# Performance work log

Measured on AMD Instinct MI355X. Metric: run time of the kernel, lower is better.

## Reference

```python
import jax, jax.numpy as jnp
import numpy as np

HIDDEN = 64
N_IN = 5
N_APP = 4
DT = 0.1
EPS = 1e-5  # torch LayerNorm default
N_HEAD_TYPES = 5  # p, q1, q3, q5, q7


def _layernorm(x, w, b):
    mu = jnp.mean(x, axis=-1, keepdims=True)
    var = jnp.mean((x - mu) ** 2, axis=-1, keepdims=True)
    return (x - mu) * jax.lax.rsqrt(var + EPS) * w + b


def setup_inputs() -> dict:
    key = jax.random.key(0)
    ks = jax.random.split(key, 8)
    B, T = 4096, 2048
    x = jax.random.normal(ks[0], (B, T, N_IN), dtype=jnp.float32)
    # xavier_uniform for rec_weights
    lim_rec = float(np.sqrt(6.0 / (HIDDEN + HIDDEN)))
    W_rec = jax.random.uniform(ks[1], (HIDDEN, HIDDEN), jnp.float32, -lim_rec, lim_rec)
    # nn.Linear default init: U(-1/sqrt(fan_in), 1/sqrt(fan_in))
    lim_in = float(np.sqrt(1.0 / N_IN))
    W_in = jax.random.uniform(ks[2], (N_IN, HIDDEN), jnp.float32, -lim_in, lim_in)
    b_in = jax.random.uniform(ks[3], (HIDDEN,), jnp.float32, -lim_in, lim_in)
    tau_param = jnp.ones((HIDDEN,), jnp.float32)
    ln1_w = jnp.ones((HIDDEN,), jnp.float32)
    ln1_b = jnp.zeros((HIDDEN,), jnp.float32)
    ln2_w = jnp.ones((HIDDEN,), jnp.float32)
    ln2_b = jnp.zeros((HIDDEN,), jnp.float32)
    lim_h = float(np.sqrt(1.0 / HIDDEN))
    head_W = jax.random.uniform(ks[4], (N_HEAD_TYPES, N_APP, HIDDEN), jnp.float32, -lim_h, lim_h)
    head_b = jax.random.uniform(ks[5], (N_HEAD_TYPES, N_APP), jnp.float32, -lim_h, lim_h)
    return {"x": x, "W_in": W_in, "b_in": b_in, "tau_param": tau_param,
            "W_rec": W_rec, "ln1_w": ln1_w, "ln1_b": ln1_b,
            "ln2_w": ln2_w, "ln2_b": ln2_b, "head_W": head_W, "head_b": head_b}


def reference(x, W_in, b_in, tau_param, W_rec, ln1_w, ln1_b, ln2_w, ln2_b, head_W, head_b):
    B = x.shape[0]
    tau = jax.nn.softplus(tau_param)  # (H,)
    # precompute the input projection for all timesteps: (T, B, H)
    xw = jnp.einsum('bts,sh->tbh', x, W_in) + b_in

    def step(h, xt):
        f = jnp.tanh(_layernorm(xt + h @ W_rec, ln1_w, ln1_b))
        h = jnp.clip(h + (-h / tau + f) * DT, -10.0, 10.0)
        return h, None

    h0 = jnp.zeros((B, HIDDEN), x.dtype)
    h, _ = jax.lax.scan(step, h0, xw)
    h = _layernorm(h, ln2_w, ln2_b)
    # stacked heads: row 0 = p_out, rows 1..4 = q1, q3, q5, q7  -> (5, B, n_app)
    out = jnp.einsum('bh,kah->kba', h, head_W) + head_b[:, None, :]
    return out
```

## Files before the change

kernel.cpp:

```cpp
#include <hip/hip_runtime.h>

#define HIDDEN  64
#define T_STEPS 2048
#define N_INPUT 5
#define DT      0.1f
#define LN_EPS  1e-5f
#define ROWS    16
#define TANH_K  2.885390081777927f

typedef short bf16x8 __attribute__((ext_vector_type(8)));
typedef float f32x4  __attribute__((ext_vector_type(4)));

union FragU { uint4 u4; unsigned int u[4]; unsigned short us[8]; bf16x8 v; };

__device__ __forceinline__ unsigned short bf16_trunc(float f) {
    return (unsigned short)(__float_as_uint(f) >> 16);
}
__device__ __forceinline__ float bf16_hi_f32(float f) {
    return __uint_as_float(__float_as_uint(f) & 0xFFFF0000u);
}
__device__ __forceinline__ unsigned int pack_hi2(float f0, float f1) {
    return __builtin_amdgcn_perm(__float_as_uint(f1), __float_as_uint(f0), 0x07060302u);
}

#define MFMA(A, B, C) __builtin_amdgcn_mfma_f32_16x16x32_bf16((A), (B), (C), 0, 0, 0)

__global__ __launch_bounds__(256, 1) void hlnn_mfma4(
    const float* __restrict__ x, const float* __restrict__ W_in,
    const float* __restrict__ b_in, const float* __restrict__ tau_param,
    const float* __restrict__ W_rec, const float* __restrict__ ln1_w,
    const float* __restrict__ ln1_b, const float* __restrict__ ln2_w,
    const float* __restrict__ ln2_b, const float* __restrict__ head_W,
    const float* __restrict__ head_b, float* __restrict__ out, int Btot)
{
    const int tid  = threadIdx.x;
    const int lane = tid & 63;
    const int w    = tid >> 6;
    const int r    = lane & 15;
    const int q    = lane >> 4;
    const int g    = blockIdx.x;

    __shared__ unsigned short hHi[ROWS][72];
    __shared__ unsigned short hLo[ROWS][72];
    __shared__ float2 stats2[ROWS][18];
    __shared__ float  hnbuf[ROWS][68];

    FragU A_hi[2], A_lo[2];
    const int cfrag = 16 * w + r;
#pragma unroll
    for (int kk = 0; kk < 2; ++kk)
#pragma unroll
        for (int j = 0; j < 8; ++j) {
            const float wv = W_rec[(kk * 32 + q * 8 + j) * HIDDEN + cfrag];
            A_hi[kk].us[j] = bf16_trunc(wv);
            A_lo[kk].us[j] = bf16_trunc(wv - bf16_hi_f32(wv));
        }
    FragU Ax_hi, Ax_lo;
#pragma unroll
    for (int j = 0; j < 8; ++j) {
        const int kg = q * 8 + j;
        const float wv = (kg < N_INPUT) ? W_in[kg * HIDDEN + cfrag] : 0.0f;
        Ax_hi.us[j] = bf16_trunc(wv);
        Ax_lo.us[j] = bf16_trunc(wv - bf16_hi_f32(wv));
    }

    float w1K[4], b1K[4], dec4[4], ln2w4[4], ln2b4[4];
    f32x4 cinit;
#pragma unroll
    for (int e = 0; e < 4; ++e) {
        const int c = 16 * w + 4 * q + e;
        w1K[e]  = ln1_w[c] * TANH_K;
        b1K[e]  = ln1_b[c] * TANH_K;
        const float tp  = tau_param[c];
        const float tau = (tp > 20.0f) ? tp : log1pf(expf(tp));
        dec4[e]  = 1.0f - DT / tau;
        ln2w4[e] = ln2_w[c];  ln2b4[e] = ln2_b[c];
        cinit[e] = b_in[c];
    }

    const float* xrow = x + (size_t)(g * ROWS + r) * T_STEPS * N_INPUT;

    f32x4 accx;
    {
        const float x0 = xrow[0], x1 = xrow[1], x2 = xrow[2], x3 = xrow[3], x4 = xrow[4];
        FragU BxH, BxL;
        BxH.u[0] = pack_hi2(x0, x1); BxH.u[1] = pack_hi2(x2, x3);
        BxH.u[2] = pack_hi2(x4, 0.f); BxH.u[3] = 0u;
        BxL.u[0] = pack_hi2(x0 - bf16_hi_f32(x0), x1 - bf16_hi_f32(x1));
        BxL.u[1] = pack_hi2(x2 - bf16_hi_f32(x2), x3 - bf16_hi_f32(x3));
        BxL.u[2] = pack_hi2(x4 - bf16_hi_f32(x4), 0.f); BxL.u[3] = 0u;
        accx = MFMA(Ax_hi.v, BxH.v, cinit);
        accx = MFMA(Ax_hi.v, BxL.v, accx);
        accx = MFMA(Ax_lo.v, BxH.v, accx);
    }

    FragU Bh[2], Bl[2];
    Bh[0].u4 = make_uint4(0,0,0,0); Bh[1].u4 = make_uint4(0,0,0,0);
    Bl[0].u4 = make_uint4(0,0,0,0); Bl[1].u4 = make_uint4(0,0,0,0);
    const f32x4 zero4 = {0.f, 0.f, 0.f, 0.f};
    float h[4] = {0.f, 0.f, 0.f, 0.f};

    for (int t = 0; t < T_STEPS; ++t) {
        const size_t toff = (size_t)((t + 1 < T_STEPS) ? (t + 1) : t) * N_INPUT;
        const float xf0 = xrow[toff + 0], xf1 = xrow[toff + 1], xf2 = xrow[toff + 2],
                    xf3 = xrow[toff + 3], xf4 = xrow[toff + 4];

        f32x4 a0 = MFMA(A_hi[0].v, Bh[0].v, accx);
        f32x4 a1 = MFMA(A_hi[1].v, Bh[1].v, zero4);
        a0 = MFMA(A_hi[0].v, Bl[0].v, a0);
        a1 = MFMA(A_hi[1].v, Bl[1].v, a1);
        a0 = MFMA(A_lo[0].v, Bh[0].v, a0);
        a1 = MFMA(A_lo[1].v, Bh[1].v, a1);
        const f32x4 acc = a0 + a1;

        const float p1 = (acc[0] + acc[1]) + (acc[2] + acc[3]);
        const float p2 = fmaf(acc[0], acc[0], fmaf(acc[1], acc[1],
                         fmaf(acc[2], acc[2], acc[3] * acc[3])));
        stats2[r][4 * w + q] = make_float2(p1, p2);
        __syncthreads();

        const float4* sp = (const float4*)&stats2[r][0];
        const float4 v0 = sp[0], v1 = sp[1], v2 = sp[2], v3 = sp[3];
        const float4 v4 = sp[4], v5 = sp[5], v6 = sp[6], v7 = sp[7];
        const float sum = (((v0.x + v0.z) + (v1.x + v1.z)) + ((v2.x + v2.z) + (v3.x + v3.z)))
                        + (((v4.x + v4.z) + (v5.x + v5.z)) + ((v6.x + v6.z) + (v7.x + v7.z)));
        const float ssq = (((v0.y + v0.w) + (v1.y + v1.w)) + ((v2.y + v2.w) + (v3.y + v3.w)))
                        + (((v4.y + v4.w) + (v5.y + v5.w)) + ((v6.y + v6.w) + (v7.y + v7.w)));

        {
            FragU nBxH, nBxL;
            nBxH.u[0] = pack_hi2(xf0, xf1); nBxH.u[1] = pack_hi2(xf2, xf3);
            nBxH.u[2] = pack_hi2(xf4, 0.f); nBxH.u[3] = 0u;
            nBxL.u[0] = pack_hi2(xf0 - bf16_hi_f32(xf0), xf1 - bf16_hi_f32(xf1));
            nBxL.u[1] = pack_hi2(xf2 - bf16_hi_f32(xf2), xf3 - bf16_hi_f32(xf3));
            nBxL.u[2] = pack_hi2(xf4 - bf16_hi_f32(xf4), 0.f); nBxL.u[3] = 0u;
            accx = MFMA(Ax_hi.v, nBxH.v, cinit);
            accx = MFMA(Ax_hi.v, nBxL.v, accx);
            accx = MFMA(Ax_lo.v, nBxH.v, accx);
        }

        const float mu   = sum * (1.0f / 64.0f);
        float var        = fmaf(mu, -mu, ssq * (1.0f / 64.0f));
        var              = fmaxf(var, 0.0f);
        const float rstd = __builtin_amdgcn_rsqf(var + LN_EPS);

#pragma unroll
        for (int e = 0; e < 4; ++e) {
            const float a1c = rstd * w1K[e];
            const float tt  = fmaf(acc[e], a1c, fmaf(-mu, a1c, b1K[e]));
            const float ex  = __builtin_amdgcn_exp2f(tt);
            const float rc  = __builtin_amdgcn_rcpf(ex + 1.0f);
            const float dtf = fmaf(DT, ex, -DT) * rc;
            const float hv  = fmaf(dec4[e], h[e], dtf);
            h[e] = fminf(fmaxf(hv, -10.0f), 10.0f);
        }

        const int c0 = 16 * w + 4 * q;
        {
            const float l0 = h[0] - bf16_hi_f32(h[0]), l1v = h[1] - bf16_hi_f32(h[1]);
            const float l2 = h[2] - bf16_hi_f32(h[2]), l3v = h[3] - bf16_hi_f32(h[3]);
            *(uint2*)&hHi[r][c0] = make_uint2(pack_hi2(h[0], h[1]), pack_hi2(h[2], h[3]));
            *(uint2*)&hLo[r][c0] = make_uint2(pack_hi2(l0, l1v),   pack_hi2(l2, l3v));
        }
        __syncthreads();

        Bh[0].u4 = *(const uint4*)&hHi[r][0 * 32 + q * 8];
        Bl[0].u4 = *(const uint4*)&hLo[r][0 * 32 + q * 8];
        Bh[1].u4 = *(const uint4*)&hHi[r][1 * 32 + q * 8];
        Bl[1].u4 = *(const uint4*)&hLo[r][1 * 32 + q * 8];
    }

    {
        const float p1 = (h[0] + h[1]) + (h[2] + h[3]);
        const float p2 = fmaf(h[0], h[0], fmaf(h[1], h[1], fmaf(h[2], h[2], h[3] * h[3])));
        __syncthreads();
        stats2[r][4 * w + q] = make_float2(p1, p2);
        __syncthreads();
        const float4* sp = (const float4*)&stats2[r][0];
        const float4 v0 = sp[0], v1 = sp[1], v2 = sp[2], v3 = sp[3];
        const float4 v4 = sp[4], v5 = sp[5], v6 = sp[6], v7 = sp[7];
        const float sum = (((v0.x + v0.z) + (v1.x + v1.z)) + ((v2.x + v2.z) + (v3.x + v3.z)))
                        + (((v4.x + v4.z) + (v5.x + v5.z)) + ((v6.x + v6.z) + (v7.x + v7.z)));
        const float ssq = (((v0.y + v0.w) + (v1.y + v1.w)) + ((v2.y + v2.w) + (v3.y + v3.w)))
                        + (((v4.y + v4.w) + (v5.y + v5.w)) + ((v6.y + v6.w) + (v7.y + v7.w)));
        const float mu   = sum * (1.0f / 64.0f);
        float var        = fmaf(mu, -mu, ssq * (1.0f / 64.0f));
        var              = fmaxf(var, 0.0f);
        const float rstd = __builtin_amdgcn_rsqf(var + LN_EPS);
        const int c0 = 16 * w + 4 * q;
        float4 hn;
        hn.x = fmaf((h[0] - mu) * rstd, ln2w4[0], ln2b4[0]);
        hn.y = fmaf((h[1] - mu) * rstd, ln2w4[1], ln2b4[1]);
        hn.z = fmaf((h[2] - mu) * rstd, ln2w4[2], ln2b4[2]);
        hn.w = fmaf((h[3] - mu) * rstd, ln2w4[3], ln2b4[3]);
        *(float4*)&hnbuf[r][c0] = hn;
    }
    __syncthreads();

    for (int o = tid; o < ROWS * 20; o += 256) {
        const int rr = o / 20, ka = o % 20;
        float p = head_b[ka];
#pragma unroll
        for (int c = 0; c < HIDDEN; ++c)
            p = fmaf(hnbuf[rr][c], head_W[ka * HIDDEN + c], p);
        const int k = ka >> 2, a = ka & 3;
        out[(size_t)k * Btot * 4 + (size_t)(g * ROWS + rr) * 4 + a] = p;
    }
}

extern "C" void kernel_launch(void* const* d_in, const int* in_sizes, int n_in,
                              void* d_out, int out_size, void* d_ws, size_t ws_size,
                              hipStream_t stream) {
    const float* x         = (const float*)d_in[0];
    const float* W_in      = (const float*)d_in[1];
    const float* b_in      = (const float*)d_in[2];
    const float* tau_param = (const float*)d_in[3];
    const float* W_rec     = (const float*)d_in[4];
    const float* ln1_w     = (const float*)d_in[5];
    const float* ln1_b     = (const float*)d_in[6];
    const float* ln2_w     = (const float*)d_in[7];
    const float* ln2_b     = (const float*)d_in[8];
    const float* head_W    = (const float*)d_in[9];
    const float* head_b    = (const float*)d_in[10];

    const int B = in_sizes[0] / (T_STEPS * N_INPUT);
    dim3 grid(B / ROWS), block(256);
    hipLaunchKernelGGL(hlnn_mfma4, grid, block, 0, stream,
                       x, W_in, b_in, tau_param, W_rec, ln1_w, ln1_b,
                       ln2_w, ln2_b, head_W, head_b, (float*)d_out, B);
}
```

Before: 1.340 ms.

## Software-pipeline input projection and split MFMA chains with lighter LDS barriers

Moves the next-step input-projection MFMAs ahead of the recurrent MFMAs and prefetches x two steps ahead. The recurrent product is split into three independent accumulator chains, which shortens the dependent MFMA chain on the critical path. Both __syncthreads calls in the loop become a raw lgkmcnt(0) wait plus s_barrier, and h fragments are read from zero-initialised LDS at the top of each step. The inline-asm barrier skips waiting on vector-memory loads, and the MFMA summation order changes slightly.

```diff
diff --git a/kernel.cpp b/kernel.cpp
--- a/kernel.cpp
+++ b/kernel.cpp
@@ -22,10 +22,13 @@
 __device__ __forceinline__ unsigned int pack_hi2(float f0, float f1) {
     return __builtin_amdgcn_perm(__float_as_uint(f1), __float_as_uint(f0), 0x07060302u);
 }
+__device__ __forceinline__ void lds_barrier() {
+    asm volatile("s_waitcnt lgkmcnt(0)\n\ts_barrier" ::: "memory");
+}
 
 #define MFMA(A, B, C) __builtin_amdgcn_mfma_f32_16x16x32_bf16((A), (B), (C), 0, 0, 0)
 
-__global__ __launch_bounds__(256, 1) void hlnn_mfma4(
+__global__ __launch_bounds__(256, 1) void hlnn_mfma5(
     const float* __restrict__ x, const float* __restrict__ W_in,
     const float* __restrict__ b_in, const float* __restrict__ tau_param,
     const float* __restrict__ W_rec, const float* __restrict__ ln1_w,
@@ -80,6 +83,12 @@
 
     const float* xrow = x + (size_t)(g * ROWS + r) * T_STEPS * N_INPUT;
 
+    for (int i = tid; i < ROWS * 36; i += 256) {
+        ((unsigned int*)hHi)[i] = 0u;
+        ((unsigned int*)hLo)[i] = 0u;
+    }
+
+    const f32x4 zero4 = {0.f, 0.f, 0.f, 0.f};
     f32x4 accx;
     {
         const float x0 = xrow[0], x1 = xrow[1], x2 = xrow[2], x3 = xrow[3], x4 = xrow[4];
@@ -93,31 +102,49 @@
         accx = MFMA(Ax_hi.v, BxL.v, accx);
         accx = MFMA(Ax_lo.v, BxH.v, accx);
     }
-
-    FragU Bh[2], Bl[2];
-    Bh[0].u4 = make_uint4(0,0,0,0); Bh[1].u4 = make_uint4(0,0,0,0);
-    Bl[0].u4 = make_uint4(0,0,0,0); Bl[1].u4 = make_uint4(0,0,0,0);
-    const f32x4 zero4 = {0.f, 0.f, 0.f, 0.f};
+    float xc0 = xrow[N_INPUT + 0], xc1 = xrow[N_INPUT + 1], xc2 = xrow[N_INPUT + 2],
+          xc3 = xrow[N_INPUT + 3], xc4 = xrow[N_INPUT + 4];
+
     float h[4] = {0.f, 0.f, 0.f, 0.f};
+    __syncthreads();
 
     for (int t = 0; t < T_STEPS; ++t) {
-        const size_t toff = (size_t)((t + 1 < T_STEPS) ? (t + 1) : t) * N_INPUT;
+        const size_t toff = (size_t)((t + 2 < T_STEPS) ? (t + 2) : (T_STEPS - 1)) * N_INPUT;
         const float xf0 = xrow[toff + 0], xf1 = xrow[toff + 1], xf2 = xrow[toff + 2],
                     xf3 = xrow[toff + 3], xf4 = xrow[toff + 4];
 
-        f32x4 a0 = MFMA(A_hi[0].v, Bh[0].v, accx);
-        f32x4 a1 = MFMA(A_hi[1].v, Bh[1].v, zero4);
-        a0 = MFMA(A_hi[0].v, Bl[0].v, a0);
-        a1 = MFMA(A_hi[1].v, Bl[1].v, a1);
-        a0 = MFMA(A_lo[0].v, Bh[0].v, a0);
-        a1 = MFMA(A_lo[1].v, Bh[1].v, a1);
-        const f32x4 acc = a0 + a1;
+        FragU Bh0, Bl0, Bh1, Bl1;
+        Bh0.u4 = *(const uint4*)&hHi[r][q * 8];
+        Bl0.u4 = *(const uint4*)&hLo[r][q * 8];
+        Bh1.u4 = *(const uint4*)&hHi[r][32 + q * 8];
+        Bl1.u4 = *(const uint4*)&hLo[r][32 + q * 8];
+
+        f32x4 accx_n;
+        {
+            FragU BxH, BxL;
+            BxH.u[0] = pack_hi2(xc0, xc1); BxH.u[1] = pack_hi2(xc2, xc3);
+            BxH.u[2] = pack_hi2(xc4, 0.f); BxH.u[3] = 0u;
+            BxL.u[0] = pack_hi2(xc0 - bf16_hi_f32(xc0), xc1 - bf16_hi_f32(xc1));
+            BxL.u[1] = pack_hi2(xc2 - bf16_hi_f32(xc2), xc3 - bf16_hi_f32(xc3));
+            BxL.u[2] = pack_hi2(xc4 - bf16_hi_f32(xc4), 0.f); BxL.u[3] = 0u;
+            accx_n = MFMA(Ax_hi.v, BxH.v, cinit);
+            accx_n = MFMA(Ax_hi.v, BxL.v, accx_n);
+            accx_n = MFMA(Ax_lo.v, BxH.v, accx_n);
+        }
+
+        f32x4 c0 = MFMA(A_hi[0].v, Bh0.v, accx);
+        f32x4 c1 = MFMA(A_hi[1].v, Bh1.v, zero4);
+        f32x4 c2 = MFMA(A_lo[0].v, Bh0.v, zero4);
+        c0 = MFMA(A_hi[0].v, Bl0.v, c0);
+        c1 = MFMA(A_hi[1].v, Bl1.v, c1);
+        c2 = MFMA(A_lo[1].v, Bh1.v, c2);
+        const f32x4 acc = (c0 + c1) + c2;
 
         const float p1 = (acc[0] + acc[1]) + (acc[2] + acc[3]);
         const float p2 = fmaf(acc[0], acc[0], fmaf(acc[1], acc[1],
                          fmaf(acc[2], acc[2], acc[3] * acc[3])));
         stats2[r][4 * w + q] = make_float2(p1, p2);
-        __syncthreads();
+        lds_barrier();
 
         const float4* sp = (const float4*)&stats2[r][0];
         const float4 v0 = sp[0], v1 = sp[1], v2 = sp[2], v3 = sp[3];
@@ -126,18 +153,6 @@
                         + (((v4.x + v4.z) + (v5.x + v5.z)) + ((v6.x + v6.z) + (v7.x + v7.z)));
         const float ssq = (((v0.y + v0.w) + (v1.y + v1.w)) + ((v2.y + v2.w) + (v3.y + v3.w)))
                         + (((v4.y + v4.w) + (v5.y + v5.w)) + ((v6.y + v6.w) + (v7.y + v7.w)));
-
-        {
-            FragU nBxH, nBxL;
-            nBxH.u[0] = pack_hi2(xf0, xf1); nBxH.u[1] = pack_hi2(xf2, xf3);
-            nBxH.u[2] = pack_hi2(xf4, 0.f); nBxH.u[3] = 0u;
-            nBxL.u[0] = pack_hi2(xf0 - bf16_hi_f32(xf0), xf1 - bf16_hi_f32(xf1));
-            nBxL.u[1] = pack_hi2(xf2 - bf16_hi_f32(xf2), xf3 - bf16_hi_f32(xf3));
-            nBxL.u[2] = pack_hi2(xf4 - bf16_hi_f32(xf4), 0.f); nBxL.u[3] = 0u;
-            accx = MFMA(Ax_hi.v, nBxH.v, cinit);
-            accx = MFMA(Ax_hi.v, nBxL.v, accx);
-            accx = MFMA(Ax_lo.v, nBxH.v, accx);
-        }
 
         const float mu   = sum * (1.0f / 64.0f);
         float var        = fmaf(mu, -mu, ssq * (1.0f / 64.0f));
@@ -155,25 +170,22 @@
             h[e] = fminf(fmaxf(hv, -10.0f), 10.0f);
         }
 
-        const int c0 = 16 * w + 4 * q;
+        const int c0w = 16 * w + 4 * q;
         {
             const float l0 = h[0] - bf16_hi_f32(h[0]), l1v = h[1] - bf16_hi_f32(h[1]);
             const float l2 = h[2] - bf16_hi_f32(h[2]), l3v = h[3] - bf16_hi_f32(h[3]);
-            *(uint2*)&hHi[r][c0] = make_uint2(pack_hi2(h[0], h[1]), pack_hi2(h[2], h[3]));
-            *(uint2*)&hLo[r][c0] = make_uint2(pack_hi2(l0, l1v),   pack_hi2(l2, l3v));
-        }
-        __syncthreads();
-
-        Bh[0].u4 = *(const uint4*)&hHi[r][0 * 32 + q * 8];
-        Bl[0].u4 = *(const uint4*)&hLo[r][0 * 32 + q * 8];
-        Bh[1].u4 = *(const uint4*)&hHi[r][1 * 32 + q * 8];
-        Bl[1].u4 = *(const uint4*)&hLo[r][1 * 32 + q * 8];
+            *(uint2*)&hHi[r][c0w] = make_uint2(pack_hi2(h[0], h[1]), pack_hi2(h[2], h[3]));
+            *(uint2*)&hLo[r][c0w] = make_uint2(pack_hi2(l0, l1v),   pack_hi2(l2, l3v));
+        }
+        lds_barrier();
+
+        accx = accx_n;
+        xc0 = xf0; xc1 = xf1; xc2 = xf2; xc3 = xf3; xc4 = xf4;
     }
 
     {
         const float p1 = (h[0] + h[1]) + (h[2] + h[3]);
         const float p2 = fmaf(h[0], h[0], fmaf(h[1], h[1], fmaf(h[2], h[2], h[3] * h[3])));
-        __syncthreads();
         stats2[r][4 * w + q] = make_float2(p1, p2);
         __syncthreads();
         const float4* sp = (const float4*)&stats2[r][0];
@@ -187,13 +199,13 @@
         float var        = fmaf(mu, -mu, ssq * (1.0f / 64.0f));
         var              = fmaxf(var, 0.0f);
         const float rstd = __builtin_amdgcn_rsqf(var + LN_EPS);
-        const int c0 = 16 * w + 4 * q;
+        const int c0w = 16 * w + 4 * q;
         float4 hn;
         hn.x = fmaf((h[0] - mu) * rstd, ln2w4[0], ln2b4[0]);
         hn.y = fmaf((h[1] - mu) * rstd, ln2w4[1], ln2b4[1]);
         hn.z = fmaf((h[2] - mu) * rstd, ln2w4[2], ln2b4[2]);
         hn.w = fmaf((h[3] - mu) * rstd, ln2w4[3], ln2b4[3]);
-        *(float4*)&hnbuf[r][c0] = hn;
+        *(float4*)&hnbuf[r][c0w] = hn;
     }
     __syncthreads();
 
@@ -225,7 +237,7 @@
 
     const int B = in_sizes[0] / (T_STEPS * N_INPUT);
     dim3 grid(B / ROWS), block(256);
-    hipLaunchKernelGGL(hlnn_mfma4, grid, block, 0, stream,
+    hipLaunchKernelGGL(hlnn_mfma5, grid, block, 0, stream,
                        x, W_in, b_in, tau_param, W_rec, ln1_w, ln1_b,
                        ln2_w, ln2_b, head_W, head_b, (float*)d_out, B);
 }
```

Result: slower. 1.463 ms (+9.1%).
